# Performance work log

Measured on AMD Instinct MI355X. Metric: run time of the kernel, lower is better.

## Reference

```python
import jax, jax.numpy as jnp
import numpy as np

N, E, D_IN, D_H, D_OUT = 100000, 3200000, 256, 256, 64
EPS = 1e-5


def spmm(row, col, w, x, n):
    # y = P @ x where P is sparse with P[row[e], col[e]] = w[e]
    return jax.ops.segment_sum(w[:, None] * x[col], row, num_segments=n)


def bn_eval(x, g, b, m, v):
    return (x - m) * jax.lax.rsqrt(v + EPS) * g + b


def setup_inputs() -> dict:
    key = jax.random.key(0)
    ks = jax.random.split(key, 8)
    return {
        "x": jax.random.normal(ks[0], (N, D_IN), jnp.float32),
        "edge_row": jax.random.randint(ks[1], (E,), 0, N),
        "edge_col": jax.random.randint(ks[2], (E,), 0, N),
        "edge_weight": jax.random.uniform(ks[3], (E,), jnp.float32),
        "W1": jax.random.normal(ks[4], (D_IN, D_H), jnp.float32) * (1.0 / np.sqrt(D_IN)),
        "b1": jnp.zeros((D_H,), jnp.float32),
        "g1": jnp.ones((D_H,), jnp.float32),
        "be1": jnp.zeros((D_H,), jnp.float32),
        "m1": jnp.zeros((D_H,), jnp.float32),
        "v1": jnp.ones((D_H,), jnp.float32),
        "W2": jax.random.normal(ks[5], (D_H, D_H), jnp.float32) * (1.0 / np.sqrt(D_H)),
        "b2": jnp.zeros((D_H,), jnp.float32),
        "g2": jnp.ones((D_H,), jnp.float32),
        "be2": jnp.zeros((D_H,), jnp.float32),
        "m2": jnp.zeros((D_H,), jnp.float32),
        "v2": jnp.ones((D_H,), jnp.float32),
        "W3": jax.random.normal(ks[6], (D_H, D_OUT), jnp.float32) * (1.0 / np.sqrt(D_H)),
        "b3": jnp.zeros((D_OUT,), jnp.float32),
    }


def reference(x, edge_row, edge_col, edge_weight,
              W1, b1, g1, be1, m1, v1,
              W2, b2, g2, be2, m2, v2,
              W3, b3):
    n = x.shape[0]
    # layer 1: linear -> BN(eval) -> SpMM -> relu  (dropout is identity in eval)
    h = x @ W1 + b1
    h = bn_eval(h, g1, be1, m1, v1)
    h = jax.nn.relu(spmm(edge_row, edge_col, edge_weight, h, n))
    # layer 2
    h = h @ W2 + b2
    h = bn_eval(h, g2, be2, m2, v2)
    h = jax.nn.relu(spmm(edge_row, edge_col, edge_weight, h, n))
    # output layer
    h = h @ W3 + b3
    h = spmm(edge_row, edge_col, edge_weight, h, n)
    return jax.nn.log_softmax(h, axis=-1)
```

## Files before the change

kernel.cpp:

```cpp
#include <hip/hip_runtime.h>

#define NN 100000
#define NE 3200000
#define NBUCK 782
#define EPB 8192
#define NCB 391

typedef __attribute__((ext_vector_type(8))) short bf16x8;
typedef __attribute__((ext_vector_type(4))) float f32x4;
typedef __attribute__((ext_vector_type(2))) float f32x2;

__device__ __forceinline__ ushort f2bf(float f) {
  unsigned u = __builtin_bit_cast(unsigned, f);
  u = (u + 0x7FFFu + ((u >> 16) & 1u)) >> 16;
  return (ushort)u;
}
__device__ __forceinline__ float bf2f(ushort h) {
  return __builtin_bit_cast(float, ((unsigned)h) << 16);
}
__device__ __forceinline__ unsigned char f2fp8(float f) {
  return (unsigned char)(__builtin_amdgcn_cvt_pk_fp8_f32(f, 0.f, 0u, false) & 0xFFu);
}
__device__ __forceinline__ float pw2w(unsigned pw) {
  return __builtin_bit_cast(float, (pw & 0x7FFFu) << 16);
}
__device__ __forceinline__ void gl2lds16(const void* g, void* s) {
  __builtin_amdgcn_global_load_lds((const __attribute__((address_space(1))) void*)g,
                                   (__attribute__((address_space(3))) void*)s, 16, 0, 0);
}

__global__ __launch_bounds__(256) void k_pc(
    const float* __restrict__ W1, const float* __restrict__ b1, const float* __restrict__ g1,
    const float* __restrict__ be1, const float* __restrict__ m1, const float* __restrict__ v1,
    const float* __restrict__ W2, const float* __restrict__ b2, const float* __restrict__ g2,
    const float* __restrict__ be2, const float* __restrict__ m2, const float* __restrict__ v2,
    const float* __restrict__ W3, const float* __restrict__ b3,
    ushort* __restrict__ W1t, ushort* __restrict__ W2t, ushort* __restrict__ W3t,
    float* __restrict__ bp1, float* __restrict__ bp2, float* __restrict__ bp3,
    const int* __restrict__ row, int* __restrict__ ghist, int* __restrict__ bcnt) {
  __shared__ int h[NBUCK];
  int bid = blockIdx.x, k = threadIdx.x;
  if (bid < 640) {
    if (bid < 256) {
      int j = bid;
      float s = g1[j] * rsqrtf(v1[j] + 1e-5f), t = be1[j] - m1[j] * s;
      if (k == 0) bp1[j] = b1[j] * s + t;
      W1t[(size_t)j * 256 + k] = f2bf(W1[(size_t)k * 256 + j] * s);
    } else if (bid < 512) {
      int j = bid - 256;
      float s = g2[j] * rsqrtf(v2[j] + 1e-5f), t = be2[j] - m2[j] * s;
      if (k == 0) bp2[j] = b2[j] * s + t;
      W2t[(size_t)j * 256 + k] = f2bf(W2[(size_t)k * 256 + j] * s);
    } else {
      int j = bid - 512;
      if (k == 0) bp3[j] = (j < 64) ? b3[j] : 0.f;
      W3t[(size_t)j * 256 + k] = f2bf((j < 64) ? W3[(size_t)k * 64 + j] : 0.f);
    }
    return;
  }
  int blk = bid - 640;
  for (int i = k; i < NBUCK; i += 256) h[i] = 0;
  __syncthreads();
  int lo = blk * EPB, hi = lo + EPB; if (hi > NE) hi = NE;
  for (int i = lo + k * 4; i < hi; i += 1024) {
    int4 r = *(const int4*)(row + i);
    atomicAdd(&h[r.x >> 7], 1);
    atomicAdd(&h[r.y >> 7], 1);
    atomicAdd(&h[r.z >> 7], 1);
    atomicAdd(&h[r.w >> 7], 1);
  }
  __syncthreads();
  for (int i = k; i < NBUCK; i += 256) {
    ghist[(size_t)i * NCB + blk] = h[i];
    if (h[i]) atomicAdd(&bcnt[i], h[i]);
  }
}

__global__ __launch_bounds__(64) void k_scan3(int* __restrict__ ghist, const int* __restrict__ bcnt,
                                              int* __restrict__ bbase) {
  int b = blockIdx.x, lane = threadIdx.x;
  int acc = 0;
  for (int i = lane; i < b; i += 64) acc += bcnt[i];
#pragma unroll
  for (int o = 32; o > 0; o >>= 1) acc += __shfl_xor(acc, o, 64);
  int carry = acc;
  if (lane == 0) bbase[b] = carry;
#pragma unroll
  for (int r = 0; r < 7; ++r) {
    int idx = r * 64 + lane;
    int v = (idx < NCB) ? ghist[(size_t)b * NCB + idx] : 0;
    int s = v;
#pragma unroll
    for (int o = 1; o < 64; o <<= 1) { int t = __shfl_up(s, o, 64); if (lane >= o) s += t; }
    if (idx < NCB) ghist[(size_t)b * NCB + idx] = carry + s - v;
    carry += __shfl(s, 63, 64);
  }
}

__global__ __launch_bounds__(256) void k_pg1(const float* __restrict__ A, const ushort* __restrict__ Bt,
                                             const float* __restrict__ bp, unsigned char* __restrict__ C,
                                             const int* __restrict__ row, const int* __restrict__ col,
                                             const float* __restrict__ w, const int* __restrict__ ghist,
                                             int2* __restrict__ bdata) {
  __shared__ char smem[32768];
  int bid = blockIdx.x;
  const int tid = threadIdx.x;
  if (bid >= 1564) {
    int* offs = (int*)smem;
    int blk = bid - 1564;
    for (int i = tid; i < NBUCK; i += 256) offs[i] = ghist[(size_t)i * NCB + blk];
    __syncthreads();
    int lo = blk * EPB, hi = lo + EPB; if (hi > NE) hi = NE;
    for (int i = lo + tid * 4; i < hi; i += 1024) {
      int4 r = *(const int4*)(row + i);
      int4 c = *(const int4*)(col + i);
      float4 ww = *(const float4*)(w + i);
      int p;
      p = atomicAdd(&offs[r.x >> 7], 1); bdata[p] = make_int2(((r.x & 127) << 17) | c.x, __float_as_int(ww.x));
      p = atomicAdd(&offs[r.y >> 7], 1); bdata[p] = make_int2(((r.y & 127) << 17) | c.y, __float_as_int(ww.y));
      p = atomicAdd(&offs[r.z >> 7], 1); bdata[p] = make_int2(((r.z & 127) << 17) | c.z, __float_as_int(ww.z));
      p = atomicAdd(&offs[r.w >> 7], 1); bdata[p] = make_int2(((r.w & 127) << 17) | c.w, __float_as_int(ww.w));
    }
    return;
  }
  char* sAb = smem;
  char* sBb = smem + 16384;
  const int lane = tid & 63;
  const int wave = tid >> 6;
  const int wm = wave >> 1, wn = wave & 1;
  const int bm = bid >> 1, bn = bid & 1;

  f32x4 acc[4][4];
#pragma unroll
  for (int a = 0; a < 4; ++a)
#pragma unroll
    for (int b = 0; b < 4; ++b) acc[a][b] = (f32x4){0.f, 0.f, 0.f, 0.f};

  const char* Bb = (const char*)Bt;
  for (int kt = 0; kt < 4; ++kt) {
#pragma unroll
    for (int it = 0; it < 4; ++it) {
      int idx = it * 2048 + tid * 8;
      int r = idx >> 6, colx = idx & 63;
      int ra = bm * 128 + r; if (ra >= NN) ra = NN - 1;
      const float* src = A + (size_t)ra * 256 + kt * 64 + colx;
      float4 u = *(const float4*)src;
      float4 v = *(const float4*)(src + 4);
      ushort4 r0; r0.x = f2bf(u.x); r0.y = f2bf(u.y); r0.z = f2bf(u.z); r0.w = f2bf(u.w);
      ushort4 r1; r1.x = f2bf(v.x); r1.y = f2bf(v.y); r1.z = f2bf(v.z); r1.w = f2bf(v.w);
      *(ushort4*)(sAb + r * 128 + colx * 2) = r0;
      *(ushort4*)(sAb + r * 128 + colx * 2 + 8) = r1;
    }
#pragma unroll
    for (int it = 0; it < 4; ++it) {
      int o = tid * 16 + it * 4096;
      int r = o >> 7, kb = o & 127;
      gl2lds16(Bb + (size_t)(bn * 128 + r) * 512 + kt * 128 + kb, sBb + o);
    }
    __syncthreads();
#pragma unroll
    for (int kk = 0; kk < 2; ++kk) {
      int kByte = kk * 64 + ((lane >> 4) << 4);
      bf16x8 af[4], bfr[4];
#pragma unroll
      for (int mi = 0; mi < 4; ++mi)
        af[mi] = *(const bf16x8*)(sAb + (wm * 64 + mi * 16 + (lane & 15)) * 128 + kByte);
#pragma unroll
      for (int ni = 0; ni < 4; ++ni)
        bfr[ni] = *(const bf16x8*)(sBb + (wn * 64 + ni * 16 + (lane & 15)) * 128 + kByte);
#pragma unroll
      for (int mi = 0; mi < 4; ++mi)
#pragma unroll
        for (int ni = 0; ni < 4; ++ni)
          acc[mi][ni] = __builtin_amdgcn_mfma_f32_16x16x32_bf16(af[mi], bfr[ni], acc[mi][ni], 0, 0, 0);
    }
    __syncthreads();
  }

  const int r0 = bm * 128 + wm * 64 + ((lane >> 4) << 2);
  const int c0 = bn * 128 + wn * 64 + (lane & 15);
#pragma unroll
  for (int ni = 0; ni < 4; ++ni) {
    int col2 = c0 + ni * 16;
    float bpv = bp[col2];
#pragma unroll
    for (int mi = 0; mi < 4; ++mi)
#pragma unroll
      for (int i = 0; i < 4; ++i) {
        int r = r0 + mi * 16 + i;
        if (r < NN) C[(size_t)r * 256 + col2] = f2fp8(acc[mi][ni][i] + bpv);
      }
  }
}

__global__ __launch_bounds__(256) void k_bsort(const int* __restrict__ bcnt, const int* __restrict__ bbase,
                                               const int2* __restrict__ bdata, unsigned* __restrict__ cw,
                                               int* __restrict__ rp) {
  __shared__ int sc[128], lpos[128];
  int b = blockIdx.x, t = threadIdx.x;
  int n = bcnt[b], base = bbase[b];
  if (t < 128) sc[t] = 0;
  __syncthreads();
  for (int i = t; i < n; i += 256) {
    int r = bdata[(size_t)base + i].x >> 17;
    atomicAdd(&sc[r], 1);
  }
  __syncthreads();
  for (int o = 1; o < 128; o <<= 1) {
    int v = (t < 128 && t >= o) ? sc[t - o] : 0;
    __syncthreads();
    if (t < 128) sc[t] += v;
    __syncthreads();
  }
  if (t < 128) {
    int excl = t ? sc[t - 1] : 0;
    lpos[t] = excl;
    int grow = b * 128 + t;
    if (grow <= NN) rp[grow] = base + excl;
  }
  __syncthreads();
  for (int i = t; i < n; i += 256) {
    int2 e = bdata[(size_t)base + i];
    int r = e.x >> 17;
    int p = atomicAdd(&lpos[r], 1);
    cw[base + p] = ((unsigned)(e.x & 0x1FFFF) << 15) | (f2bf(__int_as_float(e.y)) & 0x7FFFu);
  }
}

__global__ __launch_bounds__(256) void k_gemm(const ushort* __restrict__ A, const ushort* __restrict__ Bt,
                                              const float* __restrict__ bp, unsigned char* __restrict__ C,
                                              int M, int ldc, int ncst) {
  __shared__ ushort sA[128 * 64];
  __shared__ ushort sB[128 * 64];
  const int tid = threadIdx.x;
  const int lane = tid & 63;
  const int wave = tid >> 6;
  const int wm = wave >> 1, wn = wave & 1;
  const int bm = blockIdx.x, bn = blockIdx.y;

  f32x4 acc[4][4];
#pragma unroll
  for (int a = 0; a < 4; ++a)
#pragma unroll
    for (int b = 0; b < 4; ++b) acc[a][b] = (f32x4){0.f, 0.f, 0.f, 0.f};

  const char* Ab = (const char*)A;
  const char* Bb = (const char*)Bt;
  char* sAb = (char*)sA;
  char* sBb = (char*)sB;

  for (int kt = 0; kt < 4; ++kt) {
#pragma unroll
    for (int it = 0; it < 4; ++it) {
      int o = tid * 16 + it * 4096;
      int r = o >> 7, kb = o & 127;
      int ra = bm * 128 + r; if (ra >= M) ra = M - 1;
      gl2lds16(Ab + (size_t)ra * 512 + kt * 128 + kb, sAb + o);
      gl2lds16(Bb + (size_t)(bn * 128 + r) * 512 + kt * 128 + kb, sBb + o);
    }
    __syncthreads();
#pragma unroll
    for (int kk = 0; kk < 2; ++kk) {
      int kByte = kk * 64 + ((lane >> 4) << 4);
      bf16x8 af[4], bfr[4];
#pragma unroll
      for (int mi = 0; mi < 4; ++mi)
        af[mi] = *(const bf16x8*)(sAb + (wm * 64 + mi * 16 + (lane & 15)) * 128 + kByte);
#pragma unroll
      for (int ni = 0; ni < 4; ++ni)
        bfr[ni] = *(const bf16x8*)(sBb + (wn * 64 + ni * 16 + (lane & 15)) * 128 + kByte);
#pragma unroll
      for (int mi = 0; mi < 4; ++mi)
#pragma unroll
        for (int ni = 0; ni < 4; ++ni)
          acc[mi][ni] = __builtin_amdgcn_mfma_f32_16x16x32_bf16(af[mi], bfr[ni], acc[mi][ni], 0, 0, 0);
    }
    __syncthreads();
  }

  const int r0 = bm * 128 + wm * 64 + ((lane >> 4) << 2);
  const int c0 = bn * 128 + wn * 64 + (lane & 15);
#pragma unroll
  for (int ni = 0; ni < 4; ++ni) {
    int col = c0 + ni * 16;
    if (col >= ncst) continue;
    float bpv = bp[col];
#pragma unroll
    for (int mi = 0; mi < 4; ++mi)
#pragma unroll
      for (int i = 0; i < 4; ++i) {
        int row = r0 + mi * 16 + i;
        if (row < M) C[(size_t)row * ldc + col] = f2fp8(acc[mi][ni][i] + bpv);
      }
  }
}

__device__ __forceinline__ void gacc16(const unsigned* __restrict__ cw, int i, int rem,
                                       const char* __restrict__ Hb, f32x2& a01, f32x2& a23) {
  unsigned p[16]; unsigned g[16];
#pragma unroll
  for (int u = 0; u < 16; ++u) p[u] = cw[i + (u < rem ? u : 0)];
#pragma unroll
  for (int u = 0; u < 16; ++u) g[u] = *(const unsigned*)(Hb + ((size_t)(p[u] >> 15) << 8));
#pragma unroll
  for (int u = 0; u < 16; ++u) {
    float wf = (u < rem) ? pw2w(p[u]) : 0.f;
    f32x2 wv = {wf, wf};
    a01 += wv * __builtin_amdgcn_cvt_pk_f32_fp8(g[u], false);
    a23 += wv * __builtin_amdgcn_cvt_pk_f32_fp8(g[u], true);
  }
}

__global__ __launch_bounds__(256) void k_spmm256(const int* __restrict__ rp, const unsigned* __restrict__ cw,
                                                 const unsigned char* __restrict__ H, ushort* __restrict__ Y) {
  int node = blockIdx.x * 4 + (threadIdx.x >> 6);
  int lane = threadIdx.x & 63;
  int s = __builtin_amdgcn_readfirstlane(rp[node]);
  int e = __builtin_amdgcn_readfirstlane(rp[node + 1]);
  f32x2 a01 = {0.f, 0.f}, a23 = {0.f, 0.f};
  const char* Hb = (const char*)H + (lane << 2);
  int i = s;
  for (; i + 16 <= e; i += 16) gacc16(cw, i, 16, Hb, a01, a23);
  int rem = e - i;
  if (rem) gacc16(cw, i, rem, Hb, a01, a23);
  ushort4 o;
  o.x = f2bf(fmaxf(a01.x, 0.f)); o.y = f2bf(fmaxf(a01.y, 0.f));
  o.z = f2bf(fmaxf(a23.x, 0.f)); o.w = f2bf(fmaxf(a23.y, 0.f));
  *(ushort4*)(Y + (size_t)node * 256 + (lane << 2)) = o;
}

__device__ __forceinline__ void gacc64(const unsigned* __restrict__ cw, int i, int rem,
                                       const unsigned char* __restrict__ H, int word, int shift, float& a) {
  unsigned p[16]; unsigned g[16];
#pragma unroll
  for (int u = 0; u < 16; ++u) p[u] = cw[i + (u < rem ? u : 0)];
#pragma unroll
  for (int u = 0; u < 16; ++u)
    g[u] = *(const unsigned*)(H + ((size_t)(p[u] >> 15) << 6) + word);
#pragma unroll
  for (int u = 0; u < 16; ++u) {
    float h = __builtin_amdgcn_cvt_f32_fp8(g[u] >> shift, 0);
    a += ((u < rem) ? pw2w(p[u]) : 0.f) * h;
  }
}

__global__ __launch_bounds__(256) void k_spmm64(const int* __restrict__ rp, const unsigned* __restrict__ cw,
                                                const unsigned char* __restrict__ H, float* __restrict__ out) {
  int node = blockIdx.x * 4 + (threadIdx.x >> 6);
  int lane = threadIdx.x & 63;
  int s = __builtin_amdgcn_readfirstlane(rp[node]);
  int e = __builtin_amdgcn_readfirstlane(rp[node + 1]);
  int word = (lane >> 2) << 2;
  int shift = (lane & 3) << 3;
  float a = 0.f;
  int i = s;
  for (; i + 16 <= e; i += 16) gacc64(cw, i, 16, H, word, shift, a);
  int rem = e - i;
  if (rem) gacc64(cw, i, rem, H, word, shift, a);
  float mx = a;
#pragma unroll
  for (int o = 32; o > 0; o >>= 1) mx = fmaxf(mx, __shfl_xor(mx, o, 64));
  float ex = expf(a - mx);
  float sum = ex;
#pragma unroll
  for (int o = 32; o > 0; o >>= 1) sum += __shfl_xor(sum, o, 64);
  out[(size_t)node * 64 + lane] = (a - mx) - logf(sum);
}

extern "C" void kernel_launch(void* const* d_in, const int* in_sizes, int n_in,
                              void* d_out, int out_size, void* d_ws, size_t ws_size,
                              hipStream_t stream) {
  const float* x   = (const float*)d_in[0];
  const int* erow  = (const int*)d_in[1];
  const int* ecol  = (const int*)d_in[2];
  const float* ew  = (const float*)d_in[3];
  const float* W1  = (const float*)d_in[4];
  const float* b1  = (const float*)d_in[5];
  const float* g1  = (const float*)d_in[6];
  const float* be1 = (const float*)d_in[7];
  const float* m1  = (const float*)d_in[8];
  const float* v1  = (const float*)d_in[9];
  const float* W2  = (const float*)d_in[10];
  const float* b2  = (const float*)d_in[11];
  const float* g2  = (const float*)d_in[12];
  const float* be2 = (const float*)d_in[13];
  const float* m2  = (const float*)d_in[14];
  const float* v2  = (const float*)d_in[15];
  const float* W3  = (const float*)d_in[16];
  const float* b3  = (const float*)d_in[17];

  char* ws = (char*)d_ws;
  size_t off = 0;
  auto carve = [&](size_t bytes) -> void* {
    void* p = ws + off;
    off += (bytes + 511) & ~(size_t)511;
    return p;
  };
  int* bcnt    = (int*)carve((size_t)NBUCK * 4);
  int* bbase   = (int*)carve((size_t)NBUCK * 4);
  int* ghist   = (int*)carve((size_t)NBUCK * NCB * 4);
  int* rp      = (int*)carve((size_t)(NBUCK * 128 + 1) * 4);
  unsigned* cw = (unsigned*)carve((size_t)NE * 4);
  ushort* W1t  = (ushort*)carve(256 * 256 * 2);
  ushort* W2t  = (ushort*)carve(256 * 256 * 2);
  ushort* W3t  = (ushort*)carve(128 * 256 * 2);
  float* bp1   = (float*)carve(256 * 4);
  float* bp2   = (float*)carve(256 * 4);
  float* bp3   = (float*)carve(128 * 4);
  ushort* bufH        = (ushort*)carve((size_t)NN * 256 * 2);
  unsigned char* bufZ = (unsigned char*)carve((size_t)NN * 256);
  unsigned char* bufZ3 = (unsigned char*)carve((size_t)NN * 64);
  if (off > ws_size) return;

  int2* bdata = (int2*)bufH;

  hipMemsetAsync(bcnt, 0, (size_t)NBUCK * 4, stream);
  k_pc<<<1031, 256, 0, stream>>>(W1, b1, g1, be1, m1, v1, W2, b2, g2, be2, m2, v2, W3, b3,
                                 W1t, W2t, W3t, bp1, bp2, bp3, erow, ghist, bcnt);
  k_scan3<<<NBUCK, 64, 0, stream>>>(ghist, bcnt, bbase);
  k_pg1<<<1955, 256, 0, stream>>>(x, W1t, bp1, bufZ, erow, ecol, ew, ghist, bdata);
  k_bsort<<<NBUCK, 256, 0, stream>>>(bcnt, bbase, bdata, cw, rp);

  const int gm = (NN + 127) / 128;
  k_spmm256<<<NN / 4, 256, 0, stream>>>(rp, cw, bufZ, bufH);
  k_gemm<<<dim3(gm, 2), 256, 0, stream>>>(bufH, W2t, bp2, bufZ, NN, 256, 256);
  k_spmm256<<<NN / 4, 256, 0, stream>>>(rp, cw, bufZ, bufH);
  k_gemm<<<dim3(gm, 1), 256, 0, stream>>>(bufH, W3t, bp3, bufZ3, NN, 64, 64);
  k_spmm64<<<NN / 4, 256, 0, stream>>>(rp, cw, bufZ3, (float*)d_out);
}
```

Before: 515.5 us.

## Split fused layer-1 GEMM from edge placement; pre-convert x to bf16

Removes the combined k_pg1 kernel that did both the layer-1 GEMM (converting fp32 x to bf16 on the fly) and the edge bucket placement. x is now converted to bf16 by extra blocks in the preprocessing kernel. Placement runs as its own kernel into a dedicated bdata buffer, and layer 1 reuses the generic k_gemm on the bf16 input. This drops the fp32-load-and-convert path inside the GEMM and lets each kernel have its own block shape, at the cost of an extra bf16 write and read of x, one more launch, and losing the overlap between GEMM and placement.

```diff
diff --git a/kernel.cpp b/kernel.cpp
--- a/kernel.cpp
+++ b/kernel.cpp
@@ -37,7 +37,8 @@
     const float* __restrict__ W3, const float* __restrict__ b3,
     ushort* __restrict__ W1t, ushort* __restrict__ W2t, ushort* __restrict__ W3t,
     float* __restrict__ bp1, float* __restrict__ bp2, float* __restrict__ bp3,
-    const int* __restrict__ row, int* __restrict__ ghist, int* __restrict__ bcnt) {
+    const int* __restrict__ row, int* __restrict__ ghist, int* __restrict__ bcnt,
+    const float* __restrict__ x, ushort* __restrict__ xb) {
   __shared__ int h[NBUCK];
   int bid = blockIdx.x, k = threadIdx.x;
   if (bid < 640) {
@@ -58,6 +59,16 @@
     }
     return;
   }
+  if (bid >= 1031) {
+    size_t i = ((size_t)(bid - 1031) * 256 + k) * 8;
+    float4 u = *(const float4*)(x + i);
+    float4 v = *(const float4*)(x + i + 4);
+    ushort4 r0; r0.x = f2bf(u.x); r0.y = f2bf(u.y); r0.z = f2bf(u.z); r0.w = f2bf(u.w);
+    ushort4 r1; r1.x = f2bf(v.x); r1.y = f2bf(v.y); r1.z = f2bf(v.z); r1.w = f2bf(v.w);
+    *(ushort4*)(xb + i) = r0;
+    *(ushort4*)(xb + i + 4) = r1;
+    return;
+  }
   int blk = bid - 640;
   for (int i = k; i < NBUCK; i += 256) h[i] = 0;
   __syncthreads();
@@ -97,99 +108,23 @@
   }
 }
 
-__global__ __launch_bounds__(256) void k_pg1(const float* __restrict__ A, const ushort* __restrict__ Bt,
-                                             const float* __restrict__ bp, unsigned char* __restrict__ C,
-                                             const int* __restrict__ row, const int* __restrict__ col,
-                                             const float* __restrict__ w, const int* __restrict__ ghist,
-                                             int2* __restrict__ bdata) {
-  __shared__ char smem[32768];
-  int bid = blockIdx.x;
-  const int tid = threadIdx.x;
-  if (bid >= 1564) {
-    int* offs = (int*)smem;
-    int blk = bid - 1564;
-    for (int i = tid; i < NBUCK; i += 256) offs[i] = ghist[(size_t)i * NCB + blk];
-    __syncthreads();
-    int lo = blk * EPB, hi = lo + EPB; if (hi > NE) hi = NE;
-    for (int i = lo + tid * 4; i < hi; i += 1024) {
-      int4 r = *(const int4*)(row + i);
-      int4 c = *(const int4*)(col + i);
-      float4 ww = *(const float4*)(w + i);
-      int p;
-      p = atomicAdd(&offs[r.x >> 7], 1); bdata[p] = make_int2(((r.x & 127) << 17) | c.x, __float_as_int(ww.x));
-      p = atomicAdd(&offs[r.y >> 7], 1); bdata[p] = make_int2(((r.y & 127) << 17) | c.y, __float_as_int(ww.y));
-      p = atomicAdd(&offs[r.z >> 7], 1); bdata[p] = make_int2(((r.z & 127) << 17) | c.z, __float_as_int(ww.z));
-      p = atomicAdd(&offs[r.w >> 7], 1); bdata[p] = make_int2(((r.w & 127) << 17) | c.w, __float_as_int(ww.w));
-    }
-    return;
-  }
-  char* sAb = smem;
-  char* sBb = smem + 16384;
-  const int lane = tid & 63;
-  const int wave = tid >> 6;
-  const int wm = wave >> 1, wn = wave & 1;
-  const int bm = bid >> 1, bn = bid & 1;
-
-  f32x4 acc[4][4];
-#pragma unroll
-  for (int a = 0; a < 4; ++a)
-#pragma unroll
-    for (int b = 0; b < 4; ++b) acc[a][b] = (f32x4){0.f, 0.f, 0.f, 0.f};
-
-  const char* Bb = (const char*)Bt;
-  for (int kt = 0; kt < 4; ++kt) {
-#pragma unroll
-    for (int it = 0; it < 4; ++it) {
-      int idx = it * 2048 + tid * 8;
-      int r = idx >> 6, colx = idx & 63;
-      int ra = bm * 128 + r; if (ra >= NN) ra = NN - 1;
-      const float* src = A + (size_t)ra * 256 + kt * 64 + colx;
-      float4 u = *(const float4*)src;
-      float4 v = *(const float4*)(src + 4);
-      ushort4 r0; r0.x = f2bf(u.x); r0.y = f2bf(u.y); r0.z = f2bf(u.z); r0.w = f2bf(u.w);
-      ushort4 r1; r1.x = f2bf(v.x); r1.y = f2bf(v.y); r1.z = f2bf(v.z); r1.w = f2bf(v.w);
-      *(ushort4*)(sAb + r * 128 + colx * 2) = r0;
-      *(ushort4*)(sAb + r * 128 + colx * 2 + 8) = r1;
-    }
-#pragma unroll
-    for (int it = 0; it < 4; ++it) {
-      int o = tid * 16 + it * 4096;
-      int r = o >> 7, kb = o & 127;
-      gl2lds16(Bb + (size_t)(bn * 128 + r) * 512 + kt * 128 + kb, sBb + o);
-    }
-    __syncthreads();
-#pragma unroll
-    for (int kk = 0; kk < 2; ++kk) {
-      int kByte = kk * 64 + ((lane >> 4) << 4);
-      bf16x8 af[4], bfr[4];
-#pragma unroll
-      for (int mi = 0; mi < 4; ++mi)
-        af[mi] = *(const bf16x8*)(sAb + (wm * 64 + mi * 16 + (lane & 15)) * 128 + kByte);
-#pragma unroll
-      for (int ni = 0; ni < 4; ++ni)
-        bfr[ni] = *(const bf16x8*)(sBb + (wn * 64 + ni * 16 + (lane & 15)) * 128 + kByte);
-#pragma unroll
-      for (int mi = 0; mi < 4; ++mi)
-#pragma unroll
-        for (int ni = 0; ni < 4; ++ni)
-          acc[mi][ni] = __builtin_amdgcn_mfma_f32_16x16x32_bf16(af[mi], bfr[ni], acc[mi][ni], 0, 0, 0);
-    }
-    __syncthreads();
-  }
-
-  const int r0 = bm * 128 + wm * 64 + ((lane >> 4) << 2);
-  const int c0 = bn * 128 + wn * 64 + (lane & 15);
-#pragma unroll
-  for (int ni = 0; ni < 4; ++ni) {
-    int col2 = c0 + ni * 16;
-    float bpv = bp[col2];
-#pragma unroll
-    for (int mi = 0; mi < 4; ++mi)
-#pragma unroll
-      for (int i = 0; i < 4; ++i) {
-        int r = r0 + mi * 16 + i;
-        if (r < NN) C[(size_t)r * 256 + col2] = f2fp8(acc[mi][ni][i] + bpv);
-      }
+__global__ __launch_bounds__(256) void k_place(const int* __restrict__ row, const int* __restrict__ col,
+                                               const float* __restrict__ w, const int* __restrict__ ghist,
+                                               int2* __restrict__ bdata) {
+  __shared__ int offs[NBUCK];
+  int blk = blockIdx.x, tid = threadIdx.x;
+  for (int i = tid; i < NBUCK; i += 256) offs[i] = ghist[(size_t)i * NCB + blk];
+  __syncthreads();
+  int lo = blk * EPB, hi = lo + EPB; if (hi > NE) hi = NE;
+  for (int i = lo + tid * 4; i < hi; i += 1024) {
+    int4 r = *(const int4*)(row + i);
+    int4 c = *(const int4*)(col + i);
+    float4 ww = *(const float4*)(w + i);
+    int p;
+    p = atomicAdd(&offs[r.x >> 7], 1); bdata[p] = make_int2(((r.x & 127) << 17) | c.x, __float_as_int(ww.x));
+    p = atomicAdd(&offs[r.y >> 7], 1); bdata[p] = make_int2(((r.y & 127) << 17) | c.y, __float_as_int(ww.y));
+    p = atomicAdd(&offs[r.z >> 7], 1); bdata[p] = make_int2(((r.z & 127) << 17) | c.z, __float_as_int(ww.z));
+    p = atomicAdd(&offs[r.w >> 7], 1); bdata[p] = make_int2(((r.w & 127) << 17) | c.w, __float_as_int(ww.w));
   }
 }
 
@@ -401,6 +336,7 @@
   int* ghist   = (int*)carve((size_t)NBUCK * NCB * 4);
   int* rp      = (int*)carve((size_t)(NBUCK * 128 + 1) * 4);
   unsigned* cw = (unsigned*)carve((size_t)NE * 4);
+  int2* bdata  = (int2*)carve((size_t)NE * 8);
   ushort* W1t  = (ushort*)carve(256 * 256 * 2);
   ushort* W2t  = (ushort*)carve(256 * 256 * 2);
   ushort* W3t  = (ushort*)carve(128 * 256 * 2);
@@ -412,16 +348,15 @@
   unsigned char* bufZ3 = (unsigned char*)carve((size_t)NN * 64);
   if (off > ws_size) return;
 
-  int2* bdata = (int2*)bufH;
-
   hipMemsetAsync(bcnt, 0, (size_t)NBUCK * 4, stream);
-  k_pc<<<1031, 256, 0, stream>>>(W1, b1, g1, be1, m1, v1, W2, b2, g2, be2, m2, v2, W3, b3,
-                                 W1t, W2t, W3t, bp1, bp2, bp3, erow, ghist, bcnt);
+  k_pc<<<13531, 256, 0, stream>>>(W1, b1, g1, be1, m1, v1, W2, b2, g2, be2, m2, v2, W3, b3,
+                                  W1t, W2t, W3t, bp1, bp2, bp3, erow, ghist, bcnt, x, bufH);
   k_scan3<<<NBUCK, 64, 0, stream>>>(ghist, bcnt, bbase);
-  k_pg1<<<1955, 256, 0, stream>>>(x, W1t, bp1, bufZ, erow, ecol, ew, ghist, bdata);
+  k_place<<<NCB, 256, 0, stream>>>(erow, ecol, ew, ghist, bdata);
   k_bsort<<<NBUCK, 256, 0, stream>>>(bcnt, bbase, bdata, cw, rp);
 
   const int gm = (NN + 127) / 128;
+  k_gemm<<<dim3(gm, 2), 256, 0, stream>>>(bufH, W1t, bp1, bufZ, NN, 256, 256);
   k_spmm256<<<NN / 4, 256, 0, stream>>>(rp, cw, bufZ, bufH);
   k_gemm<<<dim3(gm, 2), 256, 0, stream>>>(bufH, W2t, bp2, bufZ, NN, 256, 256);
   k_spmm256<<<NN / 4, 256, 0, stream>>>(rp, cw, bufZ, bufH);
```

Result: no change. 525.5 us (+1.9%).
